# Kernel optimization log

Measured on AMD Instinct MI355X. Metric: run time of the kernel, lower is better.

## Reference

```python
import jax, jax.numpy as jnp
import numpy as np

B, D, C, H = 65536, 256, 128, 1024
SPLIT = D // 2           # transformed half (odd indices under 'even' mask)
NET_IN = (D - SPLIT) + C # unchanged half + cond


def setup_inputs() -> dict:
    key = jax.random.key(0)
    ks = jax.random.split(key, 10)
    s = 0.02
    return {
        "x": jax.random.normal(ks[0], (B, D), jnp.float32),
        "cond": jax.random.normal(ks[1], (B, C), jnp.float32),
        "W1": jax.random.normal(ks[2], (NET_IN, H), jnp.float32) * s,
        "b1": jnp.zeros((H,), jnp.float32),
        "W2": jax.random.normal(ks[3], (H, H), jnp.float32) * s,
        "b2": jnp.zeros((H,), jnp.float32),
        "Ws": jax.random.normal(ks[4], (H, SPLIT), jnp.float32) * s,
        "bs": jnp.zeros((SPLIT,), jnp.float32),
        "Wt": jax.random.normal(ks[5], (H, SPLIT), jnp.float32) * s,
        "bt": jnp.zeros((SPLIT,), jnp.float32),
    }


def reference(x, cond, W1, b1, W2, b2, Ws, bs, Wt, bt):
    d = x.shape[1]
    even = jnp.arange(0, d, 2)  # mask==1 -> unchanged (x1)
    odd = jnp.arange(1, d, 2)   # mask==0 -> transformed (x2)
    x1u = x[:, even]            # (B, d - d//2)
    x2u = x[:, odd]             # (B, d//2)
    h = jax.nn.relu(jnp.concatenate([x1u, cond], axis=1) @ W1 + b1)
    h = jax.nn.relu(h @ W2 + b2)
    log_s = jnp.tanh(h @ Ws + bs)
    t = h @ Wt + bt
    x2t = x2u * jnp.exp(log_s) + t
    out = jnp.zeros_like(x).at[:, even].set(x1u).at[:, odd].set(x2t)
    log_det = jnp.sum(log_s, axis=1)
    return out, log_det
```

## Files before the change

kernel.cpp:

```cpp
#include <hip/hip_runtime.h>
#include <hip/hip_bf16.h>
#include <math.h>

#define B_ROWS 65536
#define D_DIM 256
#define C_DIM 128
#define H_DIM 1024

typedef __bf16 bf16x8 __attribute__((ext_vector_type(8)));
typedef float f32x4 __attribute__((ext_vector_type(4)));
typedef short short8 __attribute__((ext_vector_type(8)));

__device__ __forceinline__ unsigned short f2bf(float f) {
    unsigned int u = __float_as_uint(f);
    u += 0x7fffu + ((u >> 16) & 1u);
    return (unsigned short)(u >> 16);
}

__device__ __forceinline__ void gl2lds16(const void* g, void* l) {
    __builtin_amdgcn_global_load_lds(
        (const __attribute__((address_space(1))) unsigned int*)g,
        (__attribute__((address_space(3))) unsigned int*)l, 16, 0, 0);
}

__device__ __forceinline__ void swizzle_mn(int id, int mtiles, int& m, int& n) {
    if ((mtiles & 7) == 0) {
        int g = id >> 6, r = id & 63;
        m = g * 8 + (r & 7);
        n = r >> 3;
    } else {
        m = id >> 3;
        n = id & 7;
    }
}

__global__ void transpose_bf16(const float* __restrict__ src, short* __restrict__ dst,
                               int R, int C, int total) {
    int tid = blockIdx.x * 256 + threadIdx.x;
    if (tid >= total) return;
    int per = R >> 3;
    int n = tid / per;
    int k0 = (tid - n * per) << 3;
    short8 o;
#pragma unroll
    for (int j = 0; j < 8; ++j) o[j] = (short)f2bf(src[(size_t)(k0 + j) * C + n]);
    *(short8*)&dst[(size_t)n * R + k0] = o;
}

__global__ void prep_b3(const float* __restrict__ bs, const float* __restrict__ bt,
                        float* __restrict__ b3) {
    int i = threadIdx.x;
    b3[i] = (i < 128) ? bs[i] : bt[i - 128];
}

__global__ __launch_bounds__(256) void gemm1_fused(
    const float* __restrict__ x, const float* __restrict__ cond,
    const short* __restrict__ Bw, const float* __restrict__ bias,
    unsigned short* __restrict__ H1, int mtiles) {
    constexpr int BK = 64, K = 256, N = 1024;
    __shared__ __align__(16) short As[128 * BK];
    __shared__ __align__(16) short Bs[128 * BK];
    const int tid = threadIdx.x;
    const int lane = tid & 63;
    const int wave = tid >> 6;
    int mt, nt;
    swizzle_mn(blockIdx.x, mtiles, mt, nt);
    const int tm = mt * 128, tn = nt * 128;
    const int mo = (wave >> 1) * 64;
    const int no = (wave & 1) * 64;

    f32x4 acc[4][4];
#pragma unroll
    for (int i = 0; i < 4; ++i)
#pragma unroll
        for (int j = 0; j < 4; ++j) acc[i][j] = f32x4{0.f, 0.f, 0.f, 0.f};

    const int srow = lane >> 3;
    const int skb = (lane & 7) ^ srow;

#pragma unroll
    for (int kc = 0; kc < K; kc += BK) {
        __syncthreads();
#pragma unroll
        for (int i = 0; i < 4; ++i) {
            int c = wave * 4 + i;
            int row = c * 8 + srow;
            int kcol = kc + skb * 8;
            float v[8];
            if (kc < 128) {
                const float4* p = (const float4*)(x + (size_t)(tm + row) * 256 + 2 * kcol);
                float4 a = p[0], b = p[1], cc = p[2], d = p[3];
                v[0]=a.x; v[1]=a.z; v[2]=b.x; v[3]=b.z; v[4]=cc.x; v[5]=cc.z; v[6]=d.x; v[7]=d.z;
            } else {
                const float4* p = (const float4*)(cond + (size_t)(tm + row) * 128 + (kcol - 128));
                float4 a = p[0], b = p[1];
                v[0]=a.x; v[1]=a.y; v[2]=a.z; v[3]=a.w; v[4]=b.x; v[5]=b.y; v[6]=b.z; v[7]=b.w;
            }
            short8 o;
#pragma unroll
            for (int j = 0; j < 8; ++j) o[j] = (short)f2bf(v[j]);
            *(short8*)&As[c * 512 + lane * 8] = o;
            gl2lds16(Bw + (size_t)(tn + row) * K + kc + skb * 8, &Bs[c * 512]);
        }
        __syncthreads();
#pragma unroll
        for (int kk = 0; kk < 2; ++kk) {
            bf16x8 af[4], bfr[4];
            int kb = kk * 4 + (lane >> 4);
#pragma unroll
            for (int t = 0; t < 4; ++t) {
                int r = mo + t * 16 + (lane & 15);
                af[t] = *(const bf16x8*)&As[r * BK + ((kb ^ (r & 7)) << 3)];
                int n = no + t * 16 + (lane & 15);
                bfr[t] = *(const bf16x8*)&Bs[n * BK + ((kb ^ (n & 7)) << 3)];
            }
#pragma unroll
            for (int i = 0; i < 4; ++i)
#pragma unroll
                for (int j = 0; j < 4; ++j)
                    acc[i][j] = __builtin_amdgcn_mfma_f32_16x16x32_bf16(
                        af[i], bfr[j], acc[i][j], 0, 0, 0);
        }
    }

#pragma unroll
    for (int j = 0; j < 4; ++j) {
        int col = tn + no + j * 16 + (lane & 15);
        float bb = bias[col];
#pragma unroll
        for (int i = 0; i < 4; ++i) {
            int row0 = tm + mo + i * 16 + ((lane >> 4) << 2);
            f32x4 v = acc[i][j];
#pragma unroll
            for (int rr = 0; rr < 4; ++rr)
                H1[(size_t)(row0 + rr) * N + col] = f2bf(fmaxf(v[rr] + bb, 0.f));
        }
    }
}

__global__ __launch_bounds__(256) void gemm_tn(
    const short* __restrict__ A, const short* __restrict__ Bw,
    const float* __restrict__ bias, unsigned short* __restrict__ Cout,
    int mtiles, int N, int K) {
    constexpr int BK = 64;
    __shared__ __align__(16) short As[128 * BK];
    __shared__ __align__(16) short Bs[128 * BK];
    const int tid = threadIdx.x;
    const int lane = tid & 63;
    const int wave = tid >> 6;
    int mt, nt;
    swizzle_mn(blockIdx.x, mtiles, mt, nt);
    const int tm = mt * 128, tn = nt * 128;
    const int mo = (wave >> 1) * 64;
    const int no = (wave & 1) * 64;

    f32x4 acc[4][4];
#pragma unroll
    for (int i = 0; i < 4; ++i)
#pragma unroll
        for (int j = 0; j < 4; ++j) acc[i][j] = f32x4{0.f, 0.f, 0.f, 0.f};

    const int srow = lane >> 3;
    const int skb = (lane & 7) ^ srow;

    for (int kc = 0; kc < K; kc += BK) {
        __syncthreads();
#pragma unroll
        for (int i = 0; i < 4; ++i) {
            int c = wave * 4 + i;
            int row = c * 8 + srow;
            gl2lds16(A + (size_t)(tm + row) * K + kc + skb * 8, &As[c * 512]);
            gl2lds16(Bw + (size_t)(tn + row) * K + kc + skb * 8, &Bs[c * 512]);
        }
        __syncthreads();
#pragma unroll
        for (int kk = 0; kk < 2; ++kk) {
            bf16x8 af[4], bfr[4];
            int kb = kk * 4 + (lane >> 4);
#pragma unroll
            for (int t = 0; t < 4; ++t) {
                int r = mo + t * 16 + (lane & 15);
                af[t] = *(const bf16x8*)&As[r * BK + ((kb ^ (r & 7)) << 3)];
                int n = no + t * 16 + (lane & 15);
                bfr[t] = *(const bf16x8*)&Bs[n * BK + ((kb ^ (n & 7)) << 3)];
            }
#pragma unroll
            for (int i = 0; i < 4; ++i)
#pragma unroll
                for (int j = 0; j < 4; ++j)
                    acc[i][j] = __builtin_amdgcn_mfma_f32_16x16x32_bf16(
                        af[i], bfr[j], acc[i][j], 0, 0, 0);
        }
    }

#pragma unroll
    for (int j = 0; j < 4; ++j) {
        int col = tn + no + j * 16 + (lane & 15);
        float bb = bias[col];
#pragma unroll
        for (int i = 0; i < 4; ++i) {
            int row0 = tm + mo + i * 16 + ((lane >> 4) << 2);
            f32x4 v = acc[i][j];
#pragma unroll
            for (int rr = 0; rr < 4; ++rr)
                Cout[(size_t)(row0 + rr) * N + col] = f2bf(fmaxf(v[rr] + bb, 0.f));
        }
    }
}

__global__ __launch_bounds__(256) void gemm3_final(
    const short* __restrict__ H2, const short* __restrict__ W3T,
    const float* __restrict__ b3, const float* __restrict__ x,
    float* __restrict__ out, float* __restrict__ logdet) {
    constexpr int BK = 64, K = 1024;
    __shared__ __align__(16) char raw[40960];
    __shared__ float rowsum[64];
    short* As = (short*)raw;
    short* Bs = (short*)(raw + 8192);
    float* Tbuf = (float*)raw;
    const int tid = threadIdx.x;
    const int lane = tid & 63;
    const int wave = tid >> 6;
    const int tm = blockIdx.x * 64;
    const int srow = lane >> 3;
    const int skb = (lane & 7) ^ srow;
    const int l15 = lane & 15;
    const int quad = lane >> 4;

    if (tid < 64) rowsum[tid] = 0.f;

    f32x4 acc[4][4];
#pragma unroll
    for (int i = 0; i < 4; ++i)
#pragma unroll
        for (int j = 0; j < 4; ++j) acc[i][j] = f32x4{0.f, 0.f, 0.f, 0.f};

    for (int kc = 0; kc < K; kc += BK) {
        __syncthreads();
#pragma unroll
        for (int i = 0; i < 10; ++i) {
            int c = wave * 10 + i;
            if (c < 8) {
                int row = c * 8 + srow;
                gl2lds16(H2 + (size_t)(tm + row) * K + kc + skb * 8, &As[c * 512]);
            } else {
                int row = (c - 8) * 8 + srow;
                gl2lds16(W3T + (size_t)row * K + kc + skb * 8, &Bs[(c - 8) * 512]);
            }
        }
        __syncthreads();
#pragma unroll
        for (int kk = 0; kk < 2; ++kk) {
            int kb = kk * 4 + quad;
            bf16x8 af[4], bfr[4];
#pragma unroll
            for (int mt = 0; mt < 4; ++mt) {
                int r = mt * 16 + l15;
                af[mt] = *(const bf16x8*)&As[r * BK + ((kb ^ (r & 7)) << 3)];
            }
#pragma unroll
            for (int nt = 0; nt < 4; ++nt) {
                int n = wave * 64 + nt * 16 + l15;
                bfr[nt] = *(const bf16x8*)&Bs[n * BK + ((kb ^ (n & 7)) << 3)];
            }
#pragma unroll
            for (int mt = 0; mt < 4; ++mt)
#pragma unroll
                for (int nt = 0; nt < 4; ++nt)
                    acc[mt][nt] = __builtin_amdgcn_mfma_f32_16x16x32_bf16(
                        af[mt], bfr[nt], acc[mt][nt], 0, 0, 0);
        }
    }

    __syncthreads();
    if (wave >= 2) {
#pragma unroll
        for (int nt = 0; nt < 4; ++nt) {
            int col = wave * 64 + nt * 16 + l15;
            float bb = b3[col];
            int cl = col - 128;
#pragma unroll
            for (int mt = 0; mt < 4; ++mt) {
#pragma unroll
                for (int rr = 0; rr < 4; ++rr) {
                    int m = mt * 16 + quad * 4 + rr;
                    Tbuf[m * 132 + cl] = acc[mt][nt][rr] + bb;
                }
            }
        }
    }
    __syncthreads();
    if (wave < 2) {
#pragma unroll
        for (int mt = 0; mt < 4; ++mt) {
#pragma unroll
            for (int rr = 0; rr < 4; ++rr) {
                int m = mt * 16 + quad * 4 + rr;
                int grow = tm + m;
                float s = 0.f;
#pragma unroll
                for (int nt = 0; nt < 4; ++nt) {
                    int j = wave * 64 + nt * 16 + l15;
                    float p = acc[mt][nt][rr] + b3[j];
                    p = fminf(fmaxf(p, -15.f), 15.f);
                    float e2 = __expf(2.f * p);
                    float ls = (e2 - 1.f) / (e2 + 1.f);
                    s += ls;
                    float tt = Tbuf[m * 132 + j];
                    float2 xv = *(const float2*)&x[(size_t)grow * 256 + 2 * j];
                    float2 ov;
                    ov.x = xv.x;
                    ov.y = xv.y * __expf(ls) + tt;
                    *(float2*)&out[(size_t)grow * 256 + 2 * j] = ov;
                }
                s += __shfl_xor(s, 1);
                s += __shfl_xor(s, 2);
                s += __shfl_xor(s, 4);
                s += __shfl_xor(s, 8);
                if (l15 == 0) atomicAdd(&rowsum[m], s);
            }
        }
    }
    __syncthreads();
    if (tid < 64) logdet[tm + tid] = rowsum[tid];
}

extern "C" void kernel_launch(void* const* d_in, const int* in_sizes, int n_in,
                              void* d_out, int out_size, void* d_ws, size_t ws_size,
                              hipStream_t stream) {
    const float* x = (const float*)d_in[0];
    const float* cond = (const float*)d_in[1];
    const float* W1 = (const float*)d_in[2];
    const float* b1 = (const float*)d_in[3];
    const float* W2 = (const float*)d_in[4];
    const float* b2 = (const float*)d_in[5];
    const float* Wsp = (const float*)d_in[6];
    const float* bs = (const float*)d_in[7];
    const float* Wtp = (const float*)d_in[8];
    const float* bt = (const float*)d_in[9];

    char* ws = (char*)d_ws;
    short* W1T = (short*)(ws);
    short* W2T = (short*)(ws + 524288ull);
    short* W3T = (short*)(ws + 2621440ull);
    float* b3  = (float*)(ws + 3145728ull);
    const size_t chunk_base = 3149824ull;

    int n_chunks = 1;
    while (n_chunks < 512) {
        size_t rp = (size_t)B_ROWS / n_chunks;
        if (chunk_base + rp * 4096ull <= ws_size) break;
        n_chunks *= 2;
    }
    const size_t RP = (size_t)B_ROWS / n_chunks;

    float* out = (float*)d_out;
    float* logdet = out + (size_t)B_ROWS * D_DIM;

    transpose_bf16<<<(32768 + 255) / 256, 256, 0, stream>>>(W1, W1T, 256, 1024, 32768);
    transpose_bf16<<<(131072 + 255) / 256, 256, 0, stream>>>(W2, W2T, 1024, 1024, 131072);
    transpose_bf16<<<(16384 + 255) / 256, 256, 0, stream>>>(Wsp, W3T, 1024, 128, 16384);
    transpose_bf16<<<(16384 + 255) / 256, 256, 0, stream>>>(Wtp, W3T + 131072, 1024, 128, 16384);
    prep_b3<<<1, 256, 0, stream>>>(bs, bt, b3);

    for (int c = 0; c < n_chunks; ++c) {
        const size_t r0 = (size_t)c * RP;
        short* H1 = (short*)(ws + chunk_base);
        short* H2 = (short*)(ws + chunk_base + 2048ull * RP);
        const int mtiles = (int)(RP / 128);

        gemm1_fused<<<mtiles * 8, 256, 0, stream>>>(
            x + r0 * D_DIM, cond + r0 * C_DIM, W1T, b1, (unsigned short*)H1, mtiles);
        gemm_tn<<<mtiles * 8, 256, 0, stream>>>(
            H1, W2T, b2, (unsigned short*)H2, mtiles, H_DIM, H_DIM);
        gemm3_final<<<(int)(RP / 64), 256, 0, stream>>>(
            H2, W3T, b3, x + r0 * D_DIM, out + r0 * D_DIM, logdet + r0);
    }
}
```

Baseline: 508.2 us.

## Add 256x256-tile eight-wave pipelined GEMM for the hidden H×H layer

Adds a new kernel for the 1024x1024 hidden layer. It uses 512 threads, 256x256 output tiles, double-buffered LDS filled by direct global-to-LDS loads, and XOR-swizzled LDS addressing. The K loop is split into four phases, each issuing part of the next tile's loads between barriers, with raised wave priority around the MFMA blocks and a grid remap that groups workgroups by XCD. The larger tile raises data reuse and the phased loads hide memory latency, but register pressure and LDS use (128 KB per block) are high, which may limit occupancy. The old kernel is kept as a fallback when the chunk row count is not a multiple of 256.

```diff
diff --git a/kernel.cpp b/kernel.cpp
--- a/kernel.cpp
+++ b/kernel.cpp
@@ -201,6 +201,158 @@
         for (int i = 0; i < 4; ++i) {
             int row0 = tm + mo + i * 16 + ((lane >> 4) << 2);
             f32x4 v = acc[i][j];
+#pragma unroll
+            for (int rr = 0; rr < 4; ++rr)
+                Cout[(size_t)(row0 + rr) * N + col] = f2bf(fmaxf(v[rr] + bb, 0.f));
+        }
+    }
+}
+
+__global__ __launch_bounds__(512, 2) void gemm2_8ph(
+    const short* __restrict__ A, const short* __restrict__ Bw,
+    const float* __restrict__ bias, unsigned short* __restrict__ Cout) {
+    constexpr int K = 1024, N = 1024, NT = 16;
+    __shared__ __align__(16) short As0[256 * 64];
+    __shared__ __align__(16) short Bs0[256 * 64];
+    __shared__ __align__(16) short As1[256 * 64];
+    __shared__ __align__(16) short Bs1[256 * 64];
+
+    const int tid = threadIdx.x;
+    const int lane = tid & 63;
+    const int wave = tid >> 6;
+    const int wm = wave >> 2;
+    const int wn = wave & 3;
+    const int l15 = lane & 15;
+    const int quad = lane >> 4;
+    const int srow = lane >> 3;
+    const int skb8 = ((lane & 7) ^ srow) << 3;
+
+    const int id = blockIdx.x, nwg = gridDim.x;
+    const int xcd = id & 7, lid = id >> 3;
+    const int q = nwg >> 3, r = nwg & 7;
+    const int wgid = (xcd < r ? xcd * (q + 1) : r * (q + 1) + (xcd - r) * q) + lid;
+    const int mt = wgid >> 2, nt = wgid & 3;
+    const size_t Abase = (size_t)(mt * 256) * K;
+    const size_t Bbase = (size_t)(nt * 256) * K;
+
+    f32x4 acc[8][4];
+#pragma unroll
+    for (int m = 0; m < 8; ++m)
+#pragma unroll
+        for (int n = 0; n < 4; ++n) acc[m][n] = f32x4{0.f, 0.f, 0.f, 0.f};
+
+    short *Ac = As0, *Bc = Bs0, *An = As1, *Bn = Bs1;
+
+    auto stage2 = [&](short* lds, const short* g, size_t rowbase, int kc, int c0, int c1) {
+        gl2lds16(g + rowbase + (size_t)(c0 * 8 + srow) * K + kc + skb8, &lds[c0 * 512]);
+        gl2lds16(g + rowbase + (size_t)(c1 * 8 + srow) * K + kc + skb8, &lds[c1 * 512]);
+    };
+    auto stageU = [&](int u, short* Ab, short* Bb, int kc) {
+        if (u == 0)      stage2(Bb, Bw, Bbase, kc, wave * 2, wave * 2 + 1);
+        else if (u == 1) stage2(Bb, Bw, Bbase, kc, 16 + wave * 2, 17 + wave * 2);
+        else if (u == 2) stage2(Ab, A, Abase, kc, wave, 16 + wave);
+        else             stage2(Ab, A, Abase, kc, 8 + wave, 24 + wave);
+    };
+
+    stageU(0, Ac, Bc, 0);
+    stageU(1, Ac, Bc, 0);
+    stageU(2, Ac, Bc, 0);
+    stageU(3, Ac, Bc, 0);
+    stageU(0, An, Bn, 64);
+    stageU(1, An, Bn, 64);
+    stageU(2, An, Bn, 64);
+    asm volatile("s_waitcnt vmcnt(6)" ::: "memory");
+    __builtin_amdgcn_sched_barrier(0);
+    __builtin_amdgcn_s_barrier();
+
+    for (int w = 0; w < NT; ++w) {
+        const int kc1 = (w + 1) << 6, kc2 = (w + 2) << 6;
+        bf16x8 bfr[4][2], af[2][2];
+
+#pragma unroll
+        for (int n = 0; n < 4; ++n) {
+            int rB = (wn << 6) + n * 16 + l15;
+#pragma unroll
+            for (int kk = 0; kk < 2; ++kk) {
+                int kb = kk * 4 + quad;
+                bfr[n][kk] = *(const bf16x8*)&Bc[rB * 64 + ((kb ^ (rB & 7)) << 3)];
+            }
+        }
+#pragma unroll
+        for (int mm = 0; mm < 2; ++mm) {
+            int rA = (wm << 7) + mm * 16 + l15;
+#pragma unroll
+            for (int kk = 0; kk < 2; ++kk) {
+                int kb = kk * 4 + quad;
+                af[mm][kk] = *(const bf16x8*)&Ac[rA * 64 + ((kb ^ (rA & 7)) << 3)];
+            }
+        }
+        if (w + 1 < NT) stageU(3, An, Bn, kc1);
+        __builtin_amdgcn_sched_barrier(0);
+        __builtin_amdgcn_s_barrier();
+        __builtin_amdgcn_sched_barrier(0);
+        __builtin_amdgcn_s_setprio(1);
+#pragma unroll
+        for (int kk = 0; kk < 2; ++kk)
+#pragma unroll
+            for (int mm = 0; mm < 2; ++mm)
+#pragma unroll
+                for (int n = 0; n < 4; ++n)
+                    acc[mm][n] = __builtin_amdgcn_mfma_f32_16x16x32_bf16(
+                        af[mm][kk], bfr[n][kk], acc[mm][n], 0, 0, 0);
+        __builtin_amdgcn_s_setprio(0);
+        __builtin_amdgcn_sched_barrier(0);
+        __builtin_amdgcn_s_barrier();
+
+#pragma unroll
+        for (int ph = 1; ph < 4; ++ph) {
+#pragma unroll
+            for (int mm = 0; mm < 2; ++mm) {
+                int rA = (wm << 7) + (ph * 2 + mm) * 16 + l15;
+#pragma unroll
+                for (int kk = 0; kk < 2; ++kk) {
+                    int kb = kk * 4 + quad;
+                    af[mm][kk] = *(const bf16x8*)&Ac[rA * 64 + ((kb ^ (rA & 7)) << 3)];
+                }
+            }
+            if (w + 2 < NT) stageU(ph - 1, Ac, Bc, kc2);
+            __builtin_amdgcn_sched_barrier(0);
+            __builtin_amdgcn_s_barrier();
+            __builtin_amdgcn_sched_barrier(0);
+            __builtin_amdgcn_s_setprio(1);
+#pragma unroll
+            for (int kk = 0; kk < 2; ++kk)
+#pragma unroll
+                for (int mm = 0; mm < 2; ++mm)
+#pragma unroll
+                    for (int n = 0; n < 4; ++n)
+                        acc[ph * 2 + mm][n] = __builtin_amdgcn_mfma_f32_16x16x32_bf16(
+                            af[mm][kk], bfr[n][kk], acc[ph * 2 + mm][n], 0, 0, 0);
+            __builtin_amdgcn_s_setprio(0);
+            if (ph == 3) {
+                if (w < NT - 2)
+                    asm volatile("s_waitcnt vmcnt(6)" ::: "memory");
+                else
+                    asm volatile("s_waitcnt vmcnt(0)" ::: "memory");
+            }
+            __builtin_amdgcn_sched_barrier(0);
+            __builtin_amdgcn_s_barrier();
+        }
+
+        short* t0 = Ac; Ac = An; An = t0;
+        short* t1 = Bc; Bc = Bn; Bn = t1;
+    }
+
+    const int tmg = mt * 256 + (wm << 7);
+    const int tng = nt * 256 + (wn << 6);
+#pragma unroll
+    for (int n = 0; n < 4; ++n) {
+        int col = tng + n * 16 + l15;
+        float bb = bias[col];
+#pragma unroll
+        for (int m = 0; m < 8; ++m) {
+            int row0 = tmg + m * 16 + (quad << 2);
+            f32x4 v = acc[m][n];
 #pragma unroll
             for (int rr = 0; rr < 4; ++rr)
                 Cout[(size_t)(row0 + rr) * N + col] = f2bf(fmaxf(v[rr] + bb, 0.f));
@@ -371,8 +523,13 @@
 
         gemm1_fused<<<mtiles * 8, 256, 0, stream>>>(
             x + r0 * D_DIM, cond + r0 * C_DIM, W1T, b1, (unsigned short*)H1, mtiles);
-        gemm_tn<<<mtiles * 8, 256, 0, stream>>>(
-            H1, W2T, b2, (unsigned short*)H2, mtiles, H_DIM, H_DIM);
+        if ((RP & 255) == 0) {
+            gemm2_8ph<<<(int)(RP / 256) * 4, 512, 0, stream>>>(
+                H1, W2T, b2, (unsigned short*)H2);
+        } else {
+            gemm_tn<<<mtiles * 8, 256, 0, stream>>>(
+                H1, W2T, b2, (unsigned short*)H2, mtiles, H_DIM, H_DIM);
+        }
         gemm3_final<<<(int)(RP / 64), 256, 0, stream>>>(
             H2, W3T, b3, x + r0 * D_DIM, out + r0 * D_DIM, logdet + r0);
     }
```

Measured after the change: 490.7 us. -3.4%, faster.
